# Kernel tuning notes

Hardware: AMD Instinct MI355X
Metric: run time of the kernel (lower is better)

Reference implementation:

```python
import jax, jax.numpy as jnp
import numpy as np
import math

B, S, E, A, H, L, V = 2, 2048, 512, 512, 8, 4, 50257
HD = A // H  # 64 per-head dim (attention_size // n_heads)
PAD = 0
EPS = 1e-5

def _sin_pe():
    pos = np.arange(S)[:, None].astype(np.float32)
    div = np.exp(np.arange(0, E, 2).astype(np.float32) * (-math.log(10000.0) / E))
    pe = np.zeros((S, E), dtype=np.float32)
    pe[:, 0::2] = np.sin(pos * div)
    pe[:, 1::2] = np.cos(pos * div)
    return jnp.asarray(pe)

PE = _sin_pe()

def setup_inputs():
    key = jax.random.key(0)
    ks = jax.random.split(key, 20)
    s = 0.02
    emb = jax.random.normal(ks[0], (V, E), jnp.float32) * s
    emb = emb.at[PAD].set(0.0)  # nn.Embedding padding_idx row is zero
    return {
        "input_ids": jax.random.randint(ks[1], (B, S), 0, V, dtype=jnp.int32),
        "attention_mask": jnp.ones((B, S), jnp.int32),
        "emb": emb,
        "Wq": jax.random.normal(ks[2], (L, H, E, HD), jnp.float32) * s,
        "Wk": jax.random.normal(ks[3], (L, H, E, HD), jnp.float32) * s,
        "Wv": jax.random.normal(ks[4], (L, H, E, HD), jnp.float32) * s,
        "Wo": jax.random.normal(ks[5], (L, A, E), jnp.float32) * s,
        "ln1_g": jnp.ones((L, E), jnp.float32),
        "ln1_b": jnp.zeros((L, E), jnp.float32),
        "ln2_g": jnp.ones((L, E), jnp.float32),
        "ln2_b": jnp.zeros((L, E), jnp.float32),
        "ff_w1": jax.random.normal(ks[6], (L, E, 4 * E), jnp.float32) * s,
        "ff_b1": jnp.zeros((L, 4 * E), jnp.float32),
        "ff_w2": jax.random.normal(ks[7], (L, 4 * E, E), jnp.float32) * s,
        "ff_b2": jnp.zeros((L, E), jnp.float32),
        "lnf_g": jnp.ones((E,), jnp.float32),
        "lnf_b": jnp.zeros((E,), jnp.float32),
        "Wout": jax.random.normal(ks[8], (E, V), jnp.float32) * s,
        "bout": jnp.zeros((V,), jnp.float32),
    }

def _ln(x, g, b):
    m = jnp.mean(x, axis=-1, keepdims=True)
    v = jnp.mean((x - m) ** 2, axis=-1, keepdims=True)
    return (x - m) / jnp.sqrt(v + EPS) * g + b

def reference(input_ids, attention_mask, emb, Wq, Wk, Wv, Wo, ln1_g, ln1_b, ln2_g, ln2_b, ff_w1, ff_b1, ff_w2, ff_b2, lnf_g, lnf_b, Wout, bout):
    # mask: padding (attention_mask==0) broadcast over queries, OR causal upper triangle
    pad = (attention_mask == 0)[:, None, :]                  # [B,1,S]
    causal = jnp.triu(jnp.ones((S, S), bool), 1)             # [S,S]
    mask = (pad | causal)[:, None, :, :]                     # [B,1,S,S]
    x = emb[input_ids] + PE[None, :S]                        # [B,S,E]
    scale = 1.0 / math.sqrt(HD)

    def block(x, p):
        wq, wk, wv, wo, g1, b1, g2, b2, w1, c1, w2, c2 = p
        xn = _ln(x, g1, b1)
        q = jnp.einsum('bse,hed->bhsd', xn, wq)
        k = jnp.einsum('bse,hed->bhsd', xn, wk)
        v = jnp.einsum('bse,hed->bhsd', xn, wv)
        scores = jnp.einsum('bhsd,bhtd->bhst', q, k) * scale  # masked_fill(-inf) then /sqrt(dk) == mask after scale
        scores = jnp.where(mask, -jnp.inf, scores)
        p_attn = jax.nn.softmax(scores, axis=-1)
        attn = jnp.einsum('bhst,bhtd->bhsd', p_attn, v)
        attn = attn.transpose(0, 2, 1, 3).reshape(B, S, A)    # concat heads
        x = x + attn @ wo                                     # residual + out proj (no bias)
        xn2 = _ln(x, g2, b2)
        h = jax.nn.gelu(xn2 @ w1 + c1, approximate=False)     # nn.GELU default (erf)
        x = x + h @ w2 + c2
        return x, None

    params = (Wq, Wk, Wv, Wo, ln1_g, ln1_b, ln2_g, ln2_b, ff_w1, ff_b1, ff_w2, ff_b2)
    x, _ = jax.lax.scan(block, x, params)
    return _ln(x, lnf_g, lnf_b) @ Wout + bout                 # [B,S,V]
```

## Files before the change

### kernel.cpp

```cpp
#include <hip/hip_runtime.h>
#include <math.h>

#define BB 2
#define SS 2048
#define EE 512
#define HH 8
#define HD 64
#define LL 4
#define VV 50257
#define NTOK (BB*SS)
#define VPAD2 50432

typedef __bf16 bf16_t;
typedef bf16_t bf16x8 __attribute__((ext_vector_type(8)));
typedef float  f32x4  __attribute__((ext_vector_type(4)));

__device__ __forceinline__ void gload_lds16(const void* g, void* l) {
  __builtin_amdgcn_global_load_lds(
      (const __attribute__((address_space(1))) void*)g,
      (__attribute__((address_space(3))) void*)l, 16, 0, 0);
}

__global__ __launch_bounds__(256) void embed_kernel(const int* __restrict__ ids,
                                                    const float* __restrict__ emb,
                                                    float* __restrict__ x) {
  int idx = blockIdx.x * 256 + threadIdx.x;
  int e   = idx & (EE - 1);
  int tok = idx >> 9;
  int s   = tok & (SS - 1);
  int id  = ids[tok];
  float freq = expf((float)(e & ~1) * -0.01798894604f);
  float ang  = (float)s * freq;
  float pe   = (e & 1) ? cosf(ang) : sinf(ang);
  x[idx] = emb[(size_t)id * EE + e] + pe;
}

__global__ __launch_bounds__(256) void ln_kernel(const float* __restrict__ in,
                                                 bf16_t* __restrict__ out,
                                                 const float* __restrict__ g,
                                                 const float* __restrict__ b) {
  int wv = threadIdx.x >> 6, lane = threadIdx.x & 63;
  int row = blockIdx.x * 4 + wv;
  const float4* r = reinterpret_cast<const float4*>(in + (size_t)row * EE) + lane * 2;
  float4 v0 = r[0], v1 = r[1];
  float s = v0.x + v0.y + v0.z + v0.w + v1.x + v1.y + v1.z + v1.w;
#pragma unroll
  for (int o = 32; o > 0; o >>= 1) s += __shfl_xor(s, o);
  float mean = s * (1.f / EE);
  float d0 = v0.x-mean, d1 = v0.y-mean, d2 = v0.z-mean, d3 = v0.w-mean;
  float d4 = v1.x-mean, d5 = v1.y-mean, d6 = v1.z-mean, d7 = v1.w-mean;
  float var = d0*d0+d1*d1+d2*d2+d3*d3+d4*d4+d5*d5+d6*d6+d7*d7;
#pragma unroll
  for (int o = 32; o > 0; o >>= 1) var += __shfl_xor(var, o);
  float inv = rsqrtf(var * (1.f / EE) + 1e-5f);
  const float4* gp = reinterpret_cast<const float4*>(g) + lane * 2;
  const float4* bp = reinterpret_cast<const float4*>(b) + lane * 2;
  float4 g0 = gp[0], g1 = gp[1], b0 = bp[0], b1 = bp[1];
  bf16_t tmp[8];
  tmp[0] = (bf16_t)(d0*inv*g0.x + b0.x); tmp[1] = (bf16_t)(d1*inv*g0.y + b0.y);
  tmp[2] = (bf16_t)(d2*inv*g0.z + b0.z); tmp[3] = (bf16_t)(d3*inv*g0.w + b0.w);
  tmp[4] = (bf16_t)(d4*inv*g1.x + b1.x); tmp[5] = (bf16_t)(d5*inv*g1.y + b1.y);
  tmp[6] = (bf16_t)(d6*inv*g1.z + b1.z); tmp[7] = (bf16_t)(d7*inv*g1.w + b1.w);
  *reinterpret_cast<bf16x8*>(out + (size_t)row * EE + lane * 8) = *reinterpret_cast<bf16x8*>(tmp);
}

__device__ __forceinline__ void transpose_tile(const float* __restrict__ ip,
                                               bf16_t* __restrict__ op,
                                               int k0, int n0, int ldin, int ldout,
                                               int Nvalid, float* T) {
  int t = threadIdx.x;
  int r = t >> 2, cb = (t & 3) * 16;
#pragma unroll
  for (int i = 0; i < 16; i++) {
    int n = n0 + cb + i;
    T[r * 65 + cb + i] = (n < Nvalid) ? ip[(size_t)(k0 + r) * ldin + n] : 0.f;
  }
  __syncthreads();
  bf16_t tmp[16];
#pragma unroll
  for (int i = 0; i < 16; i++) tmp[i] = (bf16_t)T[(cb + i) * 65 + r];
  bf16_t* o = op + (size_t)(n0 + r) * ldout + k0 + cb;
  *reinterpret_cast<bf16x8*>(o)     = *reinterpret_cast<bf16x8*>(&tmp[0]);
  *reinterpret_cast<bf16x8*>(o + 8) = *reinterpret_cast<bf16x8*>(&tmp[8]);
}

__global__ __launch_bounds__(256) void wconv_kernel(const float* __restrict__ in,
                                                    bf16_t* __restrict__ out,
                                                    int ldin, int ldout, int Nvalid,
                                                    long zin, long zout) {
  __shared__ float T[64 * 65];
  transpose_tile(in + (size_t)blockIdx.z * zin, out + (size_t)blockIdx.z * zout,
                 blockIdx.x * 64, blockIdx.y * 64, ldin, ldout, Nvalid, T);
}

__global__ __launch_bounds__(256) void wconv_qkv_kernel(const float* __restrict__ Wq,
                                                        const float* __restrict__ Wk,
                                                        const float* __restrict__ Wv,
                                                        bf16_t* __restrict__ out) {
  __shared__ float T[64 * 65];
  int z = blockIdx.z;
  int l = z / 24, rem = z % 24, sec = rem >> 3, h = rem & 7;
  const float* W = sec == 0 ? Wq : (sec == 1 ? Wk : Wv);
  const float* ip = W + (size_t)(l * 8 + h) * (EE * HD);
  bf16_t* op = out + (size_t)l * (1536 * 512) + (size_t)(sec * 512 + h * 64) * 512;
  transpose_tile(ip, op, blockIdx.x * 64, 0, HD, EE, HD, T);
}

template<int MODE, int TM>
__global__ __launch_bounds__(256) void gemm_bf16(
    const bf16_t* __restrict__ A, const bf16_t* __restrict__ Bt,
    int M, int N, int K,
    const float* __restrict__ bias,
    float* __restrict__ Cf, bf16_t* __restrict__ Cb,
    bf16_t* __restrict__ qo, bf16_t* __restrict__ ko, bf16_t* __restrict__ vo) {
  constexpr int MI = TM / 32;
  __shared__ __align__(16) bf16_t As[TM * 64];
  __shared__ __align__(16) bf16_t Bs[128 * 64];
  int tid = threadIdx.x, lane = tid & 63, w = tid >> 6;
  int lr = lane & 15, lg = lane >> 4;
  int m0 = blockIdx.y * TM, n0 = blockIdx.x * 128;
  f32x4 acc[MI][4];
#pragma unroll
  for (int i = 0; i < MI; i++)
#pragma unroll
    for (int j = 0; j < 4; j++) acc[i][j] = (f32x4){0.f, 0.f, 0.f, 0.f};
  int wr = w >> 1, wc = w & 1;

  const bf16_t* Abase = A  + (size_t)(m0 + lr) * K + lg * 8;
  const bf16_t* Bbase = Bt + (size_t)(n0 + lr) * K + lg * 8;

  for (int k0 = 0; k0 < K; k0 += 64) {
#pragma unroll
    for (int i = 0; i < MI; i++) {
      int c = w * MI + i;
      gload_lds16(Abase + (size_t)(c >> 1) * 16 * K + k0 + (c & 1) * 32,
                  (char*)As + c * 1024);
    }
#pragma unroll
    for (int i = 0; i < 4; i++) {
      int c = w * 4 + i;
      gload_lds16(Bbase + (size_t)(c >> 1) * 16 * K + k0 + (c & 1) * 32,
                  (char*)Bs + c * 1024);
    }
    __syncthreads();
#pragma unroll
    for (int kk = 0; kk < 2; kk++) {
      bf16x8 afr[MI], bfr[4];
#pragma unroll
      for (int mi = 0; mi < MI; mi++)
        afr[mi] = *reinterpret_cast<const bf16x8*>(
            &As[(((wr * MI + mi) << 1) + kk) * 512 + lane * 8]);
#pragma unroll
      for (int ni = 0; ni < 4; ni++)
        bfr[ni] = *reinterpret_cast<const bf16x8*>(
            &Bs[(((wc * 4 + ni) << 1) + kk) * 512 + lane * 8]);
#pragma unroll
      for (int mi = 0; mi < MI; mi++)
#pragma unroll
        for (int ni = 0; ni < 4; ni++)
          acc[mi][ni] = __builtin_amdgcn_mfma_f32_16x16x32_bf16(afr[mi], bfr[ni], acc[mi][ni], 0, 0, 0);
    }
    __syncthreads();
  }

#pragma unroll
  for (int mi = 0; mi < MI; mi++)
#pragma unroll
    for (int ni = 0; ni < 4; ni++) {
      int colg = n0 + wc * 64 + ni * 16 + lr;
#pragma unroll
      for (int j = 0; j < 4; j++) {
        int rowg = m0 + wr * (TM / 2) + mi * 16 + lg * 4 + j;
        float v = acc[mi][ni][j];
        if (MODE == 0) {
          int sec = colg >> 9, cc = colg & 511, hh = cc >> 6, dd = cc & 63;
          int bi = rowg >> 11, s = rowg & 2047;
          if (sec == 0)      qo[(((size_t)bi * HH + hh) * SS + s) * HD + dd] = (bf16_t)(v * 0.125f);
          else if (sec == 1) ko[(((size_t)bi * HH + hh) * SS + s) * HD + dd] = (bf16_t)v;
          else               vo[(((size_t)bi * HH + hh) * HD + dd) * SS + s] = (bf16_t)v;
        } else if (MODE == 1) {
          v += bias[colg];
          v = 0.5f * v * (1.f + erff(v * 0.70710678f));
          Cb[(size_t)rowg * N + colg] = (bf16_t)v;
        } else {
          if (bias) v += bias[colg];
          Cf[(size_t)rowg * EE + colg] += v;
        }
      }
    }
}

__global__ __launch_bounds__(512) void gemm256_out(
    const bf16_t* __restrict__ A, const bf16_t* __restrict__ Bt,
    const float* __restrict__ bias, float* __restrict__ C) {
  __shared__ __align__(16) bf16_t As[2][256 * 64];
  __shared__ __align__(16) bf16_t Bs[2][256 * 64];
  int tid = threadIdx.x, lane = tid & 63, w = tid >> 6;
  int lr = lane & 15, lg = lane >> 4;
  int bid = blockIdx.x;
  int n0 = (bid % 197) * 256, m0 = (bid / 197) * 256;
  int wr = w >> 2, wc = w & 3;
  f32x4 acc[8][4];
#pragma unroll
  for (int i = 0; i < 8; i++)
#pragma unroll
    for (int j = 0; j < 4; j++) acc[i][j] = (f32x4){0.f, 0.f, 0.f, 0.f};

  const bf16_t* Abase = A  + (size_t)(m0 + lr) * 512 + lg * 8;
  const bf16_t* Bbase = Bt + (size_t)(n0 + lr) * 512 + lg * 8;

  auto stage = [&](int b, int k0) {
#pragma unroll
    for (int i = 0; i < 4; i++) {
      int c = w * 4 + i;
      gload_lds16(Abase + (size_t)(c >> 1) * 16 * 512 + k0 + (c & 1) * 32,
                  (char*)&As[b][0] + c * 1024);
      gload_lds16(Bbase + (size_t)(c >> 1) * 16 * 512 + k0 + (c & 1) * 32,
                  (char*)&Bs[b][0] + c * 1024);
    }
  };

  stage(0, 0);
  stage(1, 64);
  asm volatile("s_waitcnt vmcnt(8)" ::: "memory");
  asm volatile("s_barrier" ::: "memory");

  for (int t = 0; t < 8; ++t) {
    int b = t & 1;
    bf16x8 breg[4][2];
#pragma unroll
    for (int q = 0; q < 4; q++) {
      if (q == 0) {
#pragma unroll
        for (int ni = 0; ni < 4; ni++)
#pragma unroll
          for (int kk = 0; kk < 2; kk++)
            breg[ni][kk] = *reinterpret_cast<const bf16x8*>(
                &Bs[b][(((wc * 4 + ni) << 1) + kk) * 512 + lane * 8]);
      }
      bf16x8 areg[2][2];
#pragma unroll
      for (int u = 0; u < 2; u++)
#pragma unroll
        for (int kk = 0; kk < 2; kk++)
          areg[u][kk] = *reinterpret_cast<const bf16x8*>(
              &As[b][(((wr * 8 + 2 * q + u) << 1) + kk) * 512 + lane * 8]);
      asm volatile("s_waitcnt lgkmcnt(0)" ::: "memory");
      __builtin_amdgcn_sched_barrier(0);
      __builtin_amdgcn_s_setprio(1);
#pragma unroll
      for (int u = 0; u < 2; u++)
#pragma unroll
        for (int ni = 0; ni < 4; ni++)
#pragma unroll
          for (int kk = 0; kk < 2; kk++)
            acc[2 * q + u][ni] = __builtin_amdgcn_mfma_f32_16x16x32_bf16(
                areg[u][kk], breg[ni][kk], acc[2 * q + u][ni], 0, 0, 0);
      __builtin_amdgcn_s_setprio(0);
      asm volatile("s_barrier" ::: "memory");
    }
    if (t < 6) {
      stage(b, (t + 2) << 6);
      asm volatile("s_waitcnt vmcnt(8)" ::: "memory");
      asm volatile("s_barrier" ::: "memory");
    } else if (t == 6) {
      asm volatile("s_waitcnt vmcnt(0)" ::: "memory");
      asm volatile("s_barrier" ::: "memory");
    }
  }

#pragma unroll
  for (int mi = 0; mi < 8; mi++)
#pragma unroll
    for (int ni = 0; ni < 4; ni++) {
      int colg = n0 + wc * 64 + ni * 16 + lr;
      if (colg < VV) {
        float bs = bias[colg];
#pragma unroll
        for (int j = 0; j < 4; j++) {
          int rowg = m0 + wr * 128 + mi * 16 + lg * 4 + j;
          C[(size_t)rowg * VV + colg] = acc[mi][ni][j] + bs;
        }
      }
    }
}

#define QBLK 128
#define KVB 64
__global__ __launch_bounds__(256) void attn_kernel(
    const bf16_t* __restrict__ qb,
    const bf16_t* __restrict__ kb,
    const bf16_t* __restrict__ vT,
    const int* __restrict__ amask,
    bf16_t* __restrict__ ab) {
  __shared__ bf16_t Qs[QBLK][72];
  __shared__ bf16_t Ks[KVB][72];
  __shared__ bf16_t Vs[HD][72];
  __shared__ bf16_t Ps[QBLK][72];
  __shared__ float  km[KVB];
  int tid = threadIdx.x, lane = tid & 63, w = tid >> 6;
  int lr = lane & 15, lg = lane >> 4;
  int q0 = blockIdx.x * QBLK, bh = blockIdx.y, b = bh >> 3, h = bh & 7;
  const bf16_t* Qg = qb + (size_t)bh * SS * HD;
  const bf16_t* Kg = kb + (size_t)bh * SS * HD;
  const bf16_t* Vg = vT + (size_t)bh * HD * SS;

  {
    int r = tid >> 1, c = (tid & 1) * 32;
    const uint4* s = reinterpret_cast<const uint4*>(Qg + (size_t)(q0 + r) * HD + c);
    uint4 a0 = s[0], a1 = s[1], a2 = s[2], a3 = s[3];
    *reinterpret_cast<uint4*>(&Qs[r][c])      = a0;
    *reinterpret_cast<uint4*>(&Qs[r][c + 8])  = a1;
    *reinterpret_cast<uint4*>(&Qs[r][c + 16]) = a2;
    *reinterpret_cast<uint4*>(&Qs[r][c + 24]) = a3;
  }

  f32x4 o[2][4];
  f32x4 m_run[2], l_run[2];
#pragma unroll
  for (int mq = 0; mq < 2; mq++) {
    m_run[mq] = (f32x4){-1e30f, -1e30f, -1e30f, -1e30f};
    l_run[mq] = (f32x4){0.f, 0.f, 0.f, 0.f};
#pragma unroll
    for (int nd = 0; nd < 4; nd++) o[mq][nd] = (f32x4){0.f, 0.f, 0.f, 0.f};
  }

  int ntile = (q0 >> 6) + 2;
  for (int t = 0; t < ntile; t++) {
    int kv0 = t * KVB;
    {
      int r = tid >> 2, c = (tid & 3) * 16;
      const uint4* s = reinterpret_cast<const uint4*>(Kg + (size_t)(kv0 + r) * HD + c);
      uint4 x0 = s[0], x1 = s[1];
      *reinterpret_cast<uint4*>(&Ks[r][c])     = x0;
      *reinterpret_cast<uint4*>(&Ks[r][c + 8]) = x1;
      const uint4* sv = reinterpret_cast<const uint4*>(Vg + (size_t)r * SS + kv0 + c);
      uint4 y0 = sv[0], y1 = sv[1];
      *reinterpret_cast<uint4*>(&Vs[r][c])     = y0;
      *reinterpret_cast<uint4*>(&Vs[r][c + 8]) = y1;
      if (tid < KVB) km[tid] = amask[b * SS + kv0 + tid] ? 0.f : -1e30f;
    }
    __syncthreads();

    f32x4 sc[2][4];
#pragma unroll
    for (int mq = 0; mq < 2; mq++)
#pragma unroll
      for (int ni = 0; ni < 4; ni++) sc[mq][ni] = (f32x4){0.f, 0.f, 0.f, 0.f};
#pragma unroll
    for (int kk = 0; kk < 2; kk++) {
      bf16x8 af[2], bf[4];
#pragma unroll
      for (int mq = 0; mq < 2; mq++)
        af[mq] = *reinterpret_cast<const bf16x8*>(&Qs[w * 32 + mq * 16 + lr][kk * 32 + lg * 8]);
#pragma unroll
      for (int ni = 0; ni < 4; ni++)
        bf[ni] = *reinterpret_cast<const bf16x8*>(&Ks[ni * 16 + lr][kk * 32 + lg * 8]);
#pragma unroll
      for (int mq = 0; mq < 2; mq++)
#pragma unroll
        for (int ni = 0; ni < 4; ni++)
          sc[mq][ni] = __builtin_amdgcn_mfma_f32_16x16x32_bf16(af[mq], bf[ni], sc[mq][ni], 0, 0, 0);
    }

    float kmv[4];
#pragma unroll
    for (int ni = 0; ni < 4; ni++) kmv[ni] = km[ni * 16 + lr];
#pragma unroll
    for (int mq = 0; mq < 2; mq++) {
      int qrb = q0 + w * 32 + mq * 16 + lg * 4;
#pragma unroll
      for (int ni = 0; ni < 4; ni++) {
        int kg = kv0 + ni * 16 + lr;
#pragma unroll
        for (int j = 0; j < 4; j++) {
          float s = sc[mq][ni][j] + kmv[ni];
          sc[mq][ni][j] = (kg <= qrb + j) ? s : -1e30f;
        }
      }
      f32x4 rmax = sc[mq][0];
#pragma unroll
      for (int ni = 1; ni < 4; ni++)
#pragma unroll
        for (int j = 0; j < 4; j++) rmax[j] = fmaxf(rmax[j], sc[mq][ni][j]);
#pragma unroll
      for (int msk = 1; msk <= 8; msk <<= 1)
#pragma unroll
        for (int j = 0; j < 4; j++) rmax[j] = fmaxf(rmax[j], __shfl_xor(rmax[j], msk));
      f32x4 mnew, corr;
#pragma unroll
      for (int j = 0; j < 4; j++) {
        mnew[j] = fmaxf(m_run[mq][j], rmax[j]);
        corr[j] = __expf(m_run[mq][j] - mnew[j]);
      }
      m_run[mq] = mnew;
      f32x4 rs = (f32x4){0.f, 0.f, 0.f, 0.f};
#pragma unroll
      for (int ni = 0; ni < 4; ni++) {
#pragma unroll
        for (int j = 0; j < 4; j++) {
          float p = __expf(sc[mq][ni][j] - mnew[j]);
          rs[j] += p;
          Ps[w * 32 + mq * 16 + lg * 4 + j][ni * 16 + lr] = (bf16_t)p;
        }
      }
#pragma unroll
      for (int msk = 1; msk <= 8; msk <<= 1)
#pragma unroll
        for (int j = 0; j < 4; j++) rs[j] += __shfl_xor(rs[j], msk);
#pragma unroll
      for (int j = 0; j < 4; j++) l_run[mq][j] = l_run[mq][j] * corr[j] + rs[j];
#pragma unroll
      for (int nd = 0; nd < 4; nd++) o[mq][nd] = o[mq][nd] * corr;
    }

#pragma unroll
    for (int kc = 0; kc < 2; kc++) {
      bf16x8 pa[2], vb[4];
#pragma unroll
      for (int mq = 0; mq < 2; mq++)
        pa[mq] = *reinterpret_cast<const bf16x8*>(&Ps[w * 32 + mq * 16 + lr][kc * 32 + lg * 8]);
#pragma unroll
      for (int nd = 0; nd < 4; nd++)
        vb[nd] = *reinterpret_cast<const bf16x8*>(&Vs[nd * 16 + lr][kc * 32 + lg * 8]);
#pragma unroll
      for (int mq = 0; mq < 2; mq++)
#pragma unroll
        for (int nd = 0; nd < 4; nd++)
          o[mq][nd] = __builtin_amdgcn_mfma_f32_16x16x32_bf16(pa[mq], vb[nd], o[mq][nd], 0, 0, 0);
    }
    __syncthreads();
  }

#pragma unroll
  for (int mq = 0; mq < 2; mq++) {
    f32x4 linv;
#pragma unroll
    for (int j = 0; j < 4; j++) linv[j] = 1.f / l_run[mq][j];
#pragma unroll
    for (int nd = 0; nd < 4; nd++)
#pragma unroll
      for (int j = 0; j < 4; j++) {
        int rowg = b * SS + q0 + w * 32 + mq * 16 + lg * 4 + j;
        int col = h * HD + nd * 16 + lr;
        ab[(size_t)rowg * EE + col] = (bf16_t)(o[mq][nd][j] * linv[j]);
      }
  }
}

extern "C" void kernel_launch(void* const* d_in, const int* in_sizes, int n_in,
                              void* d_out, int out_size, void* d_ws, size_t ws_size,
                              hipStream_t stream) {
  const int*   ids   = (const int*)d_in[0];
  const int*   amask = (const int*)d_in[1];
  const float* emb   = (const float*)d_in[2];
  const float* Wq    = (const float*)d_in[3];
  const float* Wk    = (const float*)d_in[4];
  const float* Wv    = (const float*)d_in[5];
  const float* Wo    = (const float*)d_in[6];
  const float* ln1g  = (const float*)d_in[7];
  const float* ln1b  = (const float*)d_in[8];
  const float* ln2g  = (const float*)d_in[9];
  const float* ln2b  = (const float*)d_in[10];
  const float* fw1   = (const float*)d_in[11];
  const float* fb1   = (const float*)d_in[12];
  const float* fw2   = (const float*)d_in[13];
  const float* fb2   = (const float*)d_in[14];
  const float* lnfg  = (const float*)d_in[15];
  const float* lnfb  = (const float*)d_in[16];
  const float* Wout  = (const float*)d_in[17];
  const float* bout  = (const float*)d_in[18];
  float* out = (float*)d_out;

  float*  x     = (float*)d_ws;
  bf16_t* xn    = (bf16_t*)((char*)d_ws + (8u << 20));
  bf16_t* WoutT = (bf16_t*)((char*)d_ws + (12u << 20));
  char* sc = (char*)d_out;
  bf16_t* qbuf = (bf16_t*)(sc);
  bf16_t* kbuf = (bf16_t*)(sc + 4194304);
  bf16_t* vTb  = (bf16_t*)(sc + 8388608);
  bf16_t* ab   = (bf16_t*)(sc + 12582912);
  bf16_t* hb   = (bf16_t*)(sc + 16777216);
  bf16_t* Wqkv = (bf16_t*)(sc + 33554432);
  bf16_t* WoT  = (bf16_t*)(sc + 39845888);
  bf16_t* W1T  = (bf16_t*)(sc + 41943040);
  bf16_t* W2T  = (bf16_t*)(sc + 50331648);

  wconv_qkv_kernel<<<dim3(8, 1, 96), 256, 0, stream>>>(Wq, Wk, Wv, Wqkv);
  wconv_kernel<<<dim3(8, 8, LL), 256, 0, stream>>>(Wo, WoT, 512, 512, 512,
                                                   512L * 512, 512L * 512);
  wconv_kernel<<<dim3(8, 32, LL), 256, 0, stream>>>(fw1, W1T, 2048, 512, 2048,
                                                    512L * 2048, 2048L * 512);
  wconv_kernel<<<dim3(32, 8, LL), 256, 0, stream>>>(fw2, W2T, 512, 2048, 512,
                                                    2048L * 512, 512L * 2048);
  wconv_kernel<<<dim3(8, VPAD2 / 64, 1), 256, 0, stream>>>(Wout, WoutT, VV, 512, VV, 0, 0);

  embed_kernel<<<NTOK * EE / 256, 256, 0, stream>>>(ids, emb, x);

  for (int l = 0; l < LL; l++) {
    ln_kernel<<<NTOK / 4, 256, 0, stream>>>(x, xn, ln1g + l * EE, ln1b + l * EE);
    gemm_bf16<0, 128><<<dim3(12, 32), 256, 0, stream>>>(xn, Wqkv + (size_t)l * 1536 * 512,
        NTOK, 1536, 512, nullptr, nullptr, nullptr, qbuf, kbuf, vTb);
    attn_kernel<<<dim3(SS / QBLK, BB * HH), 256, 0, stream>>>(qbuf, kbuf, vTb, amask, ab);
    gemm_bf16<2, 64><<<dim3(4, 64), 256, 0, stream>>>(ab, WoT + (size_t)l * 512 * 512,
        NTOK, 512, 512, nullptr, x, nullptr, nullptr, nullptr, nullptr);
    ln_kernel<<<NTOK / 4, 256, 0, stream>>>(x, xn, ln2g + l * EE, ln2b + l * EE);
    gemm_bf16<1, 128><<<dim3(16, 32), 256, 0, stream>>>(xn, W1T + (size_t)l * 2048 * 512,
        NTOK, 2048, 512, fb1 + l * 2048, nullptr, hb, nullptr, nullptr, nullptr);
    gemm_bf16<2, 64><<<dim3(4, 64), 256, 0, stream>>>(hb, W2T + (size_t)l * 512 * 2048,
        NTOK, 512, 2048, fb2 + l * EE, x, nullptr, nullptr, nullptr, nullptr);
  }
  ln_kernel<<<NTOK / 4, 256, 0, stream>>>(x, xn, lnfg, lnfb);
  gemm256_out<<<dim3(16 * (VPAD2 / 256)), 512, 0, stream>>>(xn, WoutT, bout, out);
}
```

Before: 1.545 ms.

## Keep vocab weight panel resident in LDS and stream activations through it

Rewrites the final vocab projection GEMM so each block holds a full 128x512 slice of the output weight in shared memory. It then loops over all 32 row tiles of activations, double-buffering only the A tiles, instead of re-staging both operands per 256x256 tile. Weight traffic is read once per block, and the vocab padding shrinks to a multiple of 128. The QKV and FFN1 GEMMs also switch from 128-row to 64-row tiles for more blocks. The trade-offs are a large LDS footprint (~160KB) that limits occupancy to one block per CU, and a barrier on every k-step.

```diff
diff --git a/kernel.cpp b/kernel.cpp
--- a/kernel.cpp
+++ b/kernel.cpp
@@ -9,7 +9,7 @@
 #define LL 4
 #define VV 50257
 #define NTOK (BB*SS)
-#define VPAD2 50432
+#define VPAD 50304
 
 typedef __bf16 bf16_t;
 typedef bf16_t bf16x8 __attribute__((ext_vector_type(8)));
@@ -190,99 +190,100 @@
     }
 }
 
-__global__ __launch_bounds__(512) void gemm256_out(
+__global__ __launch_bounds__(512) void gemm_vocab(
     const bf16_t* __restrict__ A, const bf16_t* __restrict__ Bt,
     const float* __restrict__ bias, float* __restrict__ C) {
-  __shared__ __align__(16) bf16_t As[2][256 * 64];
-  __shared__ __align__(16) bf16_t Bs[2][256 * 64];
+  __shared__ __align__(16) bf16_t Bp[128 * 512];
+  __shared__ __align__(16) bf16_t As[2][128 * 64];
   int tid = threadIdx.x, lane = tid & 63, w = tid >> 6;
   int lr = lane & 15, lg = lane >> 4;
-  int bid = blockIdx.x;
-  int n0 = (bid % 197) * 256, m0 = (bid / 197) * 256;
+  int n0 = blockIdx.x * 128;
   int wr = w >> 2, wc = w & 3;
-  f32x4 acc[8][4];
-#pragma unroll
-  for (int i = 0; i < 8; i++)
-#pragma unroll
-    for (int j = 0; j < 4; j++) acc[i][j] = (f32x4){0.f, 0.f, 0.f, 0.f};
-
-  const bf16_t* Abase = A  + (size_t)(m0 + lr) * 512 + lg * 8;
+
   const bf16_t* Bbase = Bt + (size_t)(n0 + lr) * 512 + lg * 8;
-
-  auto stage = [&](int b, int k0) {
-#pragma unroll
-    for (int i = 0; i < 4; i++) {
-      int c = w * 4 + i;
-      gload_lds16(Abase + (size_t)(c >> 1) * 16 * 512 + k0 + (c & 1) * 32,
-                  (char*)&As[b][0] + c * 1024);
-      gload_lds16(Bbase + (size_t)(c >> 1) * 16 * 512 + k0 + (c & 1) * 32,
-                  (char*)&Bs[b][0] + c * 1024);
+#pragma unroll
+  for (int i = 0; i < 16; i++) {
+    int c = w * 16 + i;
+    gload_lds16(Bbase + (size_t)w * 16 * 512 + i * 32, (char*)Bp + c * 1024);
+  }
+  const bf16_t* Abase = A + (size_t)lr * 512 + lg * 8;
+  auto stageA = [&](int buf, int s) {
+    int m = s >> 3, ks = s & 7;
+#pragma unroll
+    for (int i = 0; i < 2; i++) {
+      int c = w * 2 + i;
+      gload_lds16(Abase + (size_t)(m * 128 + (c >> 1) * 16) * 512 + ks * 64 + (c & 1) * 32,
+                  (char*)&As[buf][0] + c * 1024);
     }
   };
-
-  stage(0, 0);
-  stage(1, 64);
-  asm volatile("s_waitcnt vmcnt(8)" ::: "memory");
-  asm volatile("s_barrier" ::: "memory");
-
-  for (int t = 0; t < 8; ++t) {
-    int b = t & 1;
-    bf16x8 breg[4][2];
-#pragma unroll
-    for (int q = 0; q < 4; q++) {
-      if (q == 0) {
-#pragma unroll
-        for (int ni = 0; ni < 4; ni++)
+  stageA(0, 0);
+  asm volatile("s_waitcnt vmcnt(0)" ::: "memory");
+  __syncthreads();
+
+  float bs[2];
+  int col0 = n0 + (wc * 2) * 16 + lr;
+  int col1 = n0 + (wc * 2 + 1) * 16 + lr;
+  bs[0] = (col0 < VV) ? bias[col0] : 0.f;
+  bs[1] = (col1 < VV) ? bias[col1] : 0.f;
+
+  for (int m = 0; m < 32; m++) {
+    f32x4 acc[4][2];
+#pragma unroll
+    for (int i = 0; i < 4; i++)
+#pragma unroll
+      for (int j = 0; j < 2; j++) acc[i][j] = (f32x4){0.f, 0.f, 0.f, 0.f};
+
+#pragma unroll
+    for (int ks = 0; ks < 8; ks++) {
+      int s = (m << 3) + ks;
+      int buf = s & 1;
+      if (s + 1 < 256) {
+        stageA(buf ^ 1, s + 1);
+        asm volatile("s_waitcnt vmcnt(2)" ::: "memory");
+      } else {
+        asm volatile("s_waitcnt vmcnt(0)" ::: "memory");
+      }
+      asm volatile("s_barrier" ::: "memory");
+      bf16x8 af[4][2], bfr[2][2];
+#pragma unroll
+      for (int mi = 0; mi < 4; mi++)
+#pragma unroll
+        for (int kk = 0; kk < 2; kk++)
+          af[mi][kk] = *reinterpret_cast<const bf16x8*>(
+              &As[buf][(((wr * 4 + mi) << 1) + kk) * 512 + lane * 8]);
+#pragma unroll
+      for (int ni = 0; ni < 2; ni++)
+#pragma unroll
+        for (int kk = 0; kk < 2; kk++)
+          bfr[ni][kk] = *reinterpret_cast<const bf16x8*>(
+              &Bp[(((wc * 2 + ni) << 4) + (ks << 1) + kk) * 512 + lane * 8]);
+      __builtin_amdgcn_s_setprio(1);
+#pragma unroll
+      for (int mi = 0; mi < 4; mi++)
+#pragma unroll
+        for (int ni = 0; ni < 2; ni++)
 #pragma unroll
           for (int kk = 0; kk < 2; kk++)
-            breg[ni][kk] = *reinterpret_cast<const bf16x8*>(
-                &Bs[b][(((wc * 4 + ni) << 1) + kk) * 512 + lane * 8]);
-      }
-      bf16x8 areg[2][2];
-#pragma unroll
-      for (int u = 0; u < 2; u++)
-#pragma unroll
-        for (int kk = 0; kk < 2; kk++)
-          areg[u][kk] = *reinterpret_cast<const bf16x8*>(
-              &As[b][(((wr * 8 + 2 * q + u) << 1) + kk) * 512 + lane * 8]);
-      asm volatile("s_waitcnt lgkmcnt(0)" ::: "memory");
-      __builtin_amdgcn_sched_barrier(0);
-      __builtin_amdgcn_s_setprio(1);
-#pragma unroll
-      for (int u = 0; u < 2; u++)
-#pragma unroll
-        for (int ni = 0; ni < 4; ni++)
-#pragma unroll
-          for (int kk = 0; kk < 2; kk++)
-            acc[2 * q + u][ni] = __builtin_amdgcn_mfma_f32_16x16x32_bf16(
-                areg[u][kk], breg[ni][kk], acc[2 * q + u][ni], 0, 0, 0);
+            acc[mi][ni] = __builtin_amdgcn_mfma_f32_16x16x32_bf16(
+                af[mi][kk], bfr[ni][kk], acc[mi][ni], 0, 0, 0);
       __builtin_amdgcn_s_setprio(0);
       asm volatile("s_barrier" ::: "memory");
     }
-    if (t < 6) {
-      stage(b, (t + 2) << 6);
-      asm volatile("s_waitcnt vmcnt(8)" ::: "memory");
-      asm volatile("s_barrier" ::: "memory");
-    } else if (t == 6) {
-      asm volatile("s_waitcnt vmcnt(0)" ::: "memory");
-      asm volatile("s_barrier" ::: "memory");
-    }
-  }
-
-#pragma unroll
-  for (int mi = 0; mi < 8; mi++)
-#pragma unroll
-    for (int ni = 0; ni < 4; ni++) {
-      int colg = n0 + wc * 64 + ni * 16 + lr;
+
+#pragma unroll
+    for (int ni = 0; ni < 2; ni++) {
+      int colg = ni ? col1 : col0;
       if (colg < VV) {
-        float bs = bias[colg];
-#pragma unroll
-        for (int j = 0; j < 4; j++) {
-          int rowg = m0 + wr * 128 + mi * 16 + lg * 4 + j;
-          C[(size_t)rowg * VV + colg] = acc[mi][ni][j] + bs;
-        }
-      }
-    }
+#pragma unroll
+        for (int mi = 0; mi < 4; mi++)
+#pragma unroll
+          for (int j = 0; j < 4; j++) {
+            int rowg = m * 128 + wr * 64 + mi * 16 + lg * 4 + j;
+            C[(size_t)rowg * VV + colg] = acc[mi][ni][j] + bs[ni];
+          }
+      }
+    }
+  }
 }
 
 #define QBLK 128
@@ -493,23 +494,23 @@
                                                     512L * 2048, 2048L * 512);
   wconv_kernel<<<dim3(32, 8, LL), 256, 0, stream>>>(fw2, W2T, 512, 2048, 512,
                                                     2048L * 512, 512L * 2048);
-  wconv_kernel<<<dim3(8, VPAD2 / 64, 1), 256, 0, stream>>>(Wout, WoutT, VV, 512, VV, 0, 0);
+  wconv_kernel<<<dim3(8, VPAD / 64, 1), 256, 0, stream>>>(Wout, WoutT, VV, 512, VV, 0, 0);
 
   embed_kernel<<<NTOK * EE / 256, 256, 0, stream>>>(ids, emb, x);
 
   for (int l = 0; l < LL; l++) {
     ln_kernel<<<NTOK / 4, 256, 0, stream>>>(x, xn, ln1g + l * EE, ln1b + l * EE);
-    gemm_bf16<0, 128><<<dim3(12, 32), 256, 0, stream>>>(xn, Wqkv + (size_t)l * 1536 * 512,
+    gemm_bf16<0, 64><<<dim3(12, 64), 256, 0, stream>>>(xn, Wqkv + (size_t)l * 1536 * 512,
         NTOK, 1536, 512, nullptr, nullptr, nullptr, qbuf, kbuf, vTb);
     attn_kernel<<<dim3(SS / QBLK, BB * HH), 256, 0, stream>>>(qbuf, kbuf, vTb, amask, ab);
     gemm_bf16<2, 64><<<dim3(4, 64), 256, 0, stream>>>(ab, WoT + (size_t)l * 512 * 512,
         NTOK, 512, 512, nullptr, x, nullptr, nullptr, nullptr, nullptr);
     ln_kernel<<<NTOK / 4, 256, 0, stream>>>(x, xn, ln2g + l * EE, ln2b + l * EE);
-    gemm_bf16<1, 128><<<dim3(16, 32), 256, 0, stream>>>(xn, W1T + (size_t)l * 2048 * 512,
+    gemm_bf16<1, 64><<<dim3(16, 64), 256, 0, stream>>>(xn, W1T + (size_t)l * 2048 * 512,
         NTOK, 2048, 512, fb1 + l * 2048, nullptr, hb, nullptr, nullptr, nullptr);
     gemm_bf16<2, 64><<<dim3(4, 64), 256, 0, stream>>>(hb, W2T + (size_t)l * 512 * 2048,
         NTOK, 512, 2048, fb2 + l * EE, x, nullptr, nullptr, nullptr, nullptr);
   }
   ln_kernel<<<NTOK / 4, 256, 0, stream>>>(x, xn, lnfg, lnfb);
-  gemm256_out<<<dim3(16 * (VPAD2 / 256)), 512, 0, stream>>>(xn, WoutT, bout, out);
-}
+  gemm_vocab<<<dim3(VPAD / 128), 512, 0, stream>>>(xn, WoutT, bout, out);
+}
```

New measurement: 1.870 ms. 1.21x slower.

## Replace 256x256 vocab GEMM with 128x128 tiles loading B directly into registers

Applied to the files above, without the earlier changes.

Replaces the 512-thread 256x256-tile vocabulary projection kernel with a 256-thread 128x128-tile kernel. Only A is staged through LDS; each wave loads its B fragments straight from global memory into double-buffered registers. The vocab padding shrinks to a multiple of 128, which cuts wasted columns. The smaller tiles raise occupancy and drop B's LDS traffic and barriers, but lose per-block reuse and add more global reads of B and A.

```diff
diff --git a/kernel.cpp b/kernel.cpp
--- a/kernel.cpp
+++ b/kernel.cpp
@@ -9,7 +9,7 @@
 #define LL 4
 #define VV 50257
 #define NTOK (BB*SS)
-#define VPAD2 50432
+#define VPAD 50304
 
 typedef __bf16 bf16_t;
 typedef bf16_t bf16x8 __attribute__((ext_vector_type(8)));
@@ -190,87 +190,82 @@
     }
 }
 
-__global__ __launch_bounds__(512) void gemm256_out(
+__global__ __launch_bounds__(256) void gemm_vocab(
     const bf16_t* __restrict__ A, const bf16_t* __restrict__ Bt,
     const float* __restrict__ bias, float* __restrict__ C) {
-  __shared__ __align__(16) bf16_t As[2][256 * 64];
-  __shared__ __align__(16) bf16_t Bs[2][256 * 64];
+  __shared__ __align__(16) bf16_t As[2][128 * 64];
   int tid = threadIdx.x, lane = tid & 63, w = tid >> 6;
   int lr = lane & 15, lg = lane >> 4;
-  int bid = blockIdx.x;
-  int n0 = (bid % 197) * 256, m0 = (bid / 197) * 256;
-  int wr = w >> 2, wc = w & 3;
-  f32x4 acc[8][4];
-#pragma unroll
-  for (int i = 0; i < 8; i++)
+  int n0 = blockIdx.x * 128, m0 = blockIdx.y * 128;
+  int wr = w >> 1, wc = w & 1;
+  f32x4 acc[4][4];
+#pragma unroll
+  for (int i = 0; i < 4; i++)
 #pragma unroll
     for (int j = 0; j < 4; j++) acc[i][j] = (f32x4){0.f, 0.f, 0.f, 0.f};
 
   const bf16_t* Abase = A  + (size_t)(m0 + lr) * 512 + lg * 8;
-  const bf16_t* Bbase = Bt + (size_t)(n0 + lr) * 512 + lg * 8;
-
-  auto stage = [&](int b, int k0) {
+  const bf16_t* Bb    = Bt + (size_t)(n0 + wc * 64 + lr) * 512 + lg * 8;
+
+  auto stageA = [&](int buf, int k0) {
 #pragma unroll
     for (int i = 0; i < 4; i++) {
       int c = w * 4 + i;
       gload_lds16(Abase + (size_t)(c >> 1) * 16 * 512 + k0 + (c & 1) * 32,
-                  (char*)&As[b][0] + c * 1024);
-      gload_lds16(Bbase + (size_t)(c >> 1) * 16 * 512 + k0 + (c & 1) * 32,
-                  (char*)&Bs[b][0] + c * 1024);
+                  (char*)&As[buf][0] + c * 1024);
     }
   };
-
-  stage(0, 0);
-  stage(1, 64);
-  asm volatile("s_waitcnt vmcnt(8)" ::: "memory");
-  asm volatile("s_barrier" ::: "memory");
-
-  for (int t = 0; t < 8; ++t) {
-    int b = t & 1;
-    bf16x8 breg[4][2];
-#pragma unroll
-    for (int q = 0; q < 4; q++) {
-      if (q == 0) {
-#pragma unroll
-        for (int ni = 0; ni < 4; ni++)
-#pragma unroll
-          for (int kk = 0; kk < 2; kk++)
-            breg[ni][kk] = *reinterpret_cast<const bf16x8*>(
-                &Bs[b][(((wc * 4 + ni) << 1) + kk) * 512 + lane * 8]);
-      }
-      bf16x8 areg[2][2];
-#pragma unroll
-      for (int u = 0; u < 2; u++)
+  auto loadB = [&](bf16x8* dst, int k0) {
+#pragma unroll
+    for (int ni = 0; ni < 4; ni++)
+#pragma unroll
+      for (int kk = 0; kk < 2; kk++)
+        dst[ni * 2 + kk] = *reinterpret_cast<const bf16x8*>(
+            Bb + (size_t)ni * 16 * 512 + k0 + kk * 32);
+  };
+
+  bf16x8 bA[8], bB[8];
+  stageA(0, 0);
+  loadB(bA, 0);
+  asm volatile("s_waitcnt vmcnt(0)" ::: "memory");
+  __builtin_amdgcn_s_barrier();
+
+#pragma unroll
+  for (int t = 0; t < 8; t++) {
+    int cur = t & 1;
+    bf16x8* bc = (t & 1) ? bB : bA;
+    bf16x8* bn = (t & 1) ? bA : bB;
+    if (t < 7) {
+      stageA(cur ^ 1, (t + 1) << 6);
+      loadB(bn, (t + 1) << 6);
+    }
+    bf16x8 afr[4][2];
+#pragma unroll
+    for (int mi = 0; mi < 4; mi++)
+#pragma unroll
+      for (int kk = 0; kk < 2; kk++)
+        afr[mi][kk] = *reinterpret_cast<const bf16x8*>(
+            &As[cur][(((wr * 4 + mi) << 1) + kk) * 512 + lane * 8]);
+    asm volatile("s_waitcnt lgkmcnt(0)" ::: "memory");
+    __builtin_amdgcn_sched_barrier(0);
+    __builtin_amdgcn_s_setprio(1);
+#pragma unroll
+    for (int mi = 0; mi < 4; mi++)
+#pragma unroll
+      for (int ni = 0; ni < 4; ni++)
 #pragma unroll
         for (int kk = 0; kk < 2; kk++)
-          areg[u][kk] = *reinterpret_cast<const bf16x8*>(
-              &As[b][(((wr * 8 + 2 * q + u) << 1) + kk) * 512 + lane * 8]);
-      asm volatile("s_waitcnt lgkmcnt(0)" ::: "memory");
-      __builtin_amdgcn_sched_barrier(0);
-      __builtin_amdgcn_s_setprio(1);
-#pragma unroll
-      for (int u = 0; u < 2; u++)
-#pragma unroll
-        for (int ni = 0; ni < 4; ni++)
-#pragma unroll
-          for (int kk = 0; kk < 2; kk++)
-            acc[2 * q + u][ni] = __builtin_amdgcn_mfma_f32_16x16x32_bf16(
-                areg[u][kk], breg[ni][kk], acc[2 * q + u][ni], 0, 0, 0);
-      __builtin_amdgcn_s_setprio(0);
-      asm volatile("s_barrier" ::: "memory");
-    }
-    if (t < 6) {
-      stage(b, (t + 2) << 6);
+          acc[mi][ni] = __builtin_amdgcn_mfma_f32_16x16x32_bf16(
+              afr[mi][kk], bc[ni * 2 + kk], acc[mi][ni], 0, 0, 0);
+    __builtin_amdgcn_s_setprio(0);
+    if (t < 7) {
       asm volatile("s_waitcnt vmcnt(8)" ::: "memory");
-      asm volatile("s_barrier" ::: "memory");
-    } else if (t == 6) {
-      asm volatile("s_waitcnt vmcnt(0)" ::: "memory");
-      asm volatile("s_barrier" ::: "memory");
-    }
-  }
-
-#pragma unroll
-  for (int mi = 0; mi < 8; mi++)
+      __builtin_amdgcn_s_barrier();
+    }
+  }
+
+#pragma unroll
+  for (int mi = 0; mi < 4; mi++)
 #pragma unroll
     for (int ni = 0; ni < 4; ni++) {
       int colg = n0 + wc * 64 + ni * 16 + lr;
@@ -278,7 +273,7 @@
         float bs = bias[colg];
 #pragma unroll
         for (int j = 0; j < 4; j++) {
-          int rowg = m0 + wr * 128 + mi * 16 + lg * 4 + j;
+          int rowg = m0 + wr * 64 + mi * 16 + lg * 4 + j;
           C[(size_t)rowg * VV + colg] = acc[mi][ni][j] + bs;
         }
       }
@@ -493,7 +488,7 @@
                                                     512L * 2048, 2048L * 512);
   wconv_kernel<<<dim3(32, 8, LL), 256, 0, stream>>>(fw2, W2T, 512, 2048, 512,
                                                     2048L * 512, 512L * 2048);
-  wconv_kernel<<<dim3(8, VPAD2 / 64, 1), 256, 0, stream>>>(Wout, WoutT, VV, 512, VV, 0, 0);
+  wconv_kernel<<<dim3(8, VPAD / 64, 1), 256, 0, stream>>>(Wout, WoutT, VV, 512, VV, 0, 0);
 
   embed_kernel<<<NTOK * EE / 256, 256, 0, stream>>>(ids, emb, x);
 
@@ -511,5 +506,5 @@
         NTOK, 512, 2048, fb2 + l * EE, x, nullptr, nullptr, nullptr, nullptr);
   }
   ln_kernel<<<NTOK / 4, 256, 0, stream>>>(x, xn, lnfg, lnfb);
-  gemm256_out<<<dim3(16 * (VPAD2 / 256)), 512, 0, stream>>>(xn, WoutT, bout, out);
-}
+  gemm_vocab<<<dim3(VPAD / 128, 32), 256, 0, stream>>>(xn, WoutT, bout, out);
+}
```

After: 1.731 ms. 1.12x slower.

## Double-buffer attention K/V tiles via direct global-to-LDS loads

Applied to the files above, without the earlier changes.

The attention kernel now stages K and V tiles into two LDS buffers using global_load_lds. The next tile's load is issued before the current tile's compute, so it can overlap with the MFMA work. K/V are stored in a fragment-ordered, unpadded layout that lets each lane read its operand with a contiguous lane*8 index. The whole padding mask row is precomputed once into LDS. LDS use grows (double buffers plus a 2048-float mask), which may reduce occupancy, and the loop-end sync is now a manual vmcnt wait plus s_barrier.

```diff
diff --git a/kernel.cpp b/kernel.cpp
--- a/kernel.cpp
+++ b/kernel.cpp
@@ -294,10 +294,10 @@
     const int* __restrict__ amask,
     bf16_t* __restrict__ ab) {
   __shared__ bf16_t Qs[QBLK][72];
-  __shared__ bf16_t Ks[KVB][72];
-  __shared__ bf16_t Vs[HD][72];
   __shared__ bf16_t Ps[QBLK][72];
-  __shared__ float  km[KVB];
+  __shared__ __align__(16) bf16_t Ks[2][KVB * 64];
+  __shared__ __align__(16) bf16_t Vs[2][KVB * 64];
+  __shared__ float kmAll[SS];
   int tid = threadIdx.x, lane = tid & 63, w = tid >> 6;
   int lr = lane & 15, lg = lane >> 4;
   int q0 = blockIdx.x * QBLK, bh = blockIdx.y, b = bh >> 3, h = bh & 7;
@@ -314,6 +314,26 @@
     *reinterpret_cast<uint4*>(&Qs[r][c + 16]) = a2;
     *reinterpret_cast<uint4*>(&Qs[r][c + 24]) = a3;
   }
+#pragma unroll
+  for (int i = 0; i < 8; i++) {
+    int s = i * 256 + tid;
+    kmAll[s] = amask[b * SS + s] ? 0.f : -1e30f;
+  }
+
+  auto stageKV = [&](int buf, int kv0) {
+#pragma unroll
+    for (int i = 0; i < 4; i++) {
+      int c = w * 4 + i;
+      if (c < 8) {
+        gload_lds16(Kg + (size_t)(kv0 + (c >> 1) * 16 + lr) * HD + (c & 1) * 32 + lg * 8,
+                    (char*)&Ks[buf][0] + c * 1024);
+      } else {
+        int cc = c - 8;
+        gload_lds16(Vg + (size_t)((cc >> 1) * 16 + lr) * SS + kv0 + (cc & 1) * 32 + lg * 8,
+                    (char*)&Vs[buf][0] + cc * 1024);
+      }
+    }
+  };
 
   f32x4 o[2][4];
   f32x4 m_run[2], l_run[2];
@@ -325,22 +345,14 @@
     for (int nd = 0; nd < 4; nd++) o[mq][nd] = (f32x4){0.f, 0.f, 0.f, 0.f};
   }
 
+  stageKV(0, 0);
+  __syncthreads();
+
   int ntile = (q0 >> 6) + 2;
   for (int t = 0; t < ntile; t++) {
+    int buf = t & 1;
     int kv0 = t * KVB;
-    {
-      int r = tid >> 2, c = (tid & 3) * 16;
-      const uint4* s = reinterpret_cast<const uint4*>(Kg + (size_t)(kv0 + r) * HD + c);
-      uint4 x0 = s[0], x1 = s[1];
-      *reinterpret_cast<uint4*>(&Ks[r][c])     = x0;
-      *reinterpret_cast<uint4*>(&Ks[r][c + 8]) = x1;
-      const uint4* sv = reinterpret_cast<const uint4*>(Vg + (size_t)r * SS + kv0 + c);
-      uint4 y0 = sv[0], y1 = sv[1];
-      *reinterpret_cast<uint4*>(&Vs[r][c])     = y0;
-      *reinterpret_cast<uint4*>(&Vs[r][c + 8]) = y1;
-      if (tid < KVB) km[tid] = amask[b * SS + kv0 + tid] ? 0.f : -1e30f;
-    }
-    __syncthreads();
+    if (t + 1 < ntile) stageKV(buf ^ 1, kv0 + KVB);
 
     f32x4 sc[2][4];
 #pragma unroll
@@ -355,7 +367,7 @@
         af[mq] = *reinterpret_cast<const bf16x8*>(&Qs[w * 32 + mq * 16 + lr][kk * 32 + lg * 8]);
 #pragma unroll
       for (int ni = 0; ni < 4; ni++)
-        bf[ni] = *reinterpret_cast<const bf16x8*>(&Ks[ni * 16 + lr][kk * 32 + lg * 8]);
+        bf[ni] = *reinterpret_cast<const bf16x8*>(&Ks[buf][(((ni << 1) + kk)) * 512 + lane * 8]);
 #pragma unroll
       for (int mq = 0; mq < 2; mq++)
 #pragma unroll
@@ -365,7 +377,7 @@
 
     float kmv[4];
 #pragma unroll
-    for (int ni = 0; ni < 4; ni++) kmv[ni] = km[ni * 16 + lr];
+    for (int ni = 0; ni < 4; ni++) kmv[ni] = kmAll[kv0 + ni * 16 + lr];
 #pragma unroll
     for (int mq = 0; mq < 2; mq++) {
       int qrb = q0 + w * 32 + mq * 16 + lg * 4;
@@ -422,14 +434,15 @@
         pa[mq] = *reinterpret_cast<const bf16x8*>(&Ps[w * 32 + mq * 16 + lr][kc * 32 + lg * 8]);
 #pragma unroll
       for (int nd = 0; nd < 4; nd++)
-        vb[nd] = *reinterpret_cast<const bf16x8*>(&Vs[nd * 16 + lr][kc * 32 + lg * 8]);
+        vb[nd] = *reinterpret_cast<const bf16x8*>(&Vs[buf][(((nd << 1) + kc)) * 512 + lane * 8]);
 #pragma unroll
       for (int mq = 0; mq < 2; mq++)
 #pragma unroll
         for (int nd = 0; nd < 4; nd++)
           o[mq][nd] = __builtin_amdgcn_mfma_f32_16x16x32_bf16(pa[mq], vb[nd], o[mq][nd], 0, 0, 0);
     }
-    __syncthreads();
+    asm volatile("s_waitcnt vmcnt(0)" ::: "memory");
+    asm volatile("s_barrier" ::: "memory");
   }
 
 #pragma unroll
```

Result: faster. 1.513 ms (-2.0%).
